# Kernel tuning notes

Measured on AMD Instinct MI355X. Metric: run time of the kernel, lower is better.

The kernel has to match this reference:

```python
import jax, jax.numpy as jnp
import numpy as np

D = 256; NH = 8; NL = 4; NP = 4; DFF = 2048; HD = D // NH
SHAPES = [(64, 64), (32, 32), (16, 16), (8, 8)]
B = 2; LEN = sum(h * w for h, w in SHAPES)


def setup_inputs() -> dict:
    key = jax.random.key(0)
    ks = jax.random.split(key, 12)
    def w(k, shape, s=0.02):
        return jax.random.normal(k, shape, jnp.float32) * s
    starts = np.cumsum([0] + [h * w for h, w in SHAPES[:-1]])
    return {
        "src": jax.random.normal(ks[0], (B, LEN, D), jnp.float32),
        "pos": jax.random.normal(ks[1], (B, LEN, D), jnp.float32) * 0.1,
        "spatial_shapes": jnp.array(SHAPES, dtype=jnp.int32),
        "level_start_index": jnp.array(starts, dtype=jnp.int32),
        "w_value": w(ks[2], (D, D)), "b_value": jnp.zeros((D,), jnp.float32),
        "w_off": w(ks[3], (D, NH * NL * NP * 2)), "b_off": w(ks[4], (NH * NL * NP * 2,), 0.1),
        "w_attn": w(ks[5], (D, NH * NL * NP)), "b_attn": jnp.zeros((NH * NL * NP,), jnp.float32),
        "w_out": w(ks[6], (D, D)), "b_out": jnp.zeros((D,), jnp.float32),
        "w1": w(ks[7], (D, DFF)), "b1": jnp.zeros((DFF,), jnp.float32),
        "w2": w(ks[8], (DFF, D)), "b2": jnp.zeros((D,), jnp.float32),
        "g1": jnp.ones((D,), jnp.float32), "be1": jnp.zeros((D,), jnp.float32),
        "g2": jnp.ones((D,), jnp.float32), "be2": jnp.zeros((D,), jnp.float32),
    }


def _layer_norm(x, g, b):
    mu = jnp.mean(x, -1, keepdims=True)
    v = jnp.var(x, -1, keepdims=True)
    return (x - mu) * jax.lax.rsqrt(v + 1e-5) * g + b


def _reference_points(shapes):
    # torch.linspace(0.5, H-0.5, H)/H == (arange(H)+0.5)/H
    refs = []
    for H, W in shapes:
        ry = (jnp.arange(H, dtype=jnp.float32) + 0.5) / H
        rx = (jnp.arange(W, dtype=jnp.float32) + 0.5) / W
        yy, xx = jnp.meshgrid(ry, rx, indexing='ij')
        refs.append(jnp.stack([xx.ravel(), yy.ravel()], -1))
    return jnp.concatenate(refs, 0)  # (Len, 2) as (x, y)


def _ms_deform_sample(value, loc, shapes):
    # value: (B, Len, NH, HD); loc: (B, Lq, NH, NL, NP, 2) normalized [0,1]
    # Replicates torch grid_sample(bilinear, padding='zeros', align_corners=False).
    Bn, Lq = loc.shape[0], loc.shape[1]
    P = loc.shape[4]
    start = 0
    outs = []
    for lvl, (H, W) in enumerate(shapes):
        v = value[:, start:start + H * W].transpose(0, 2, 1, 3)  # (B, NH, HW, HD)
        start += H * W
        l = loc[:, :, :, lvl]                      # (B, Lq, NH, P, 2)
        x = l[..., 0] * W - 0.5
        y = l[..., 1] * H - 0.5
        x0 = jnp.floor(x); y0 = jnp.floor(y)
        dx = x - x0; dy = y - y0
        x0i = x0.astype(jnp.int32); y0i = y0.astype(jnp.int32)
        acc = None
        for xi, yi, wgt in ((x0i, y0i, (1 - dx) * (1 - dy)),
                            (x0i + 1, y0i, dx * (1 - dy)),
                            (x0i, y0i + 1, (1 - dx) * dy),
                            (x0i + 1, y0i + 1, dx * dy)):
            valid = ((xi >= 0) & (xi < W) & (yi >= 0) & (yi < H)).astype(value.dtype)
            idx = jnp.clip(yi, 0, H - 1) * W + jnp.clip(xi, 0, W - 1)  # (B, Lq, NH, P)
            idx = idx.transpose(0, 2, 1, 3).reshape(Bn, NH, Lq * P)
            g = jnp.take_along_axis(v, idx[..., None], axis=2).reshape(Bn, NH, Lq, P, HD)
            w = (wgt * valid).transpose(0, 2, 1, 3)[..., None]  # (B, NH, Lq, P, 1)
            acc = g * w if acc is None else acc + g * w
        outs.append(acc)  # (B, NH, Lq, P, HD)
    return jnp.stack(outs, 3)  # (B, NH, Lq, NL, NP, HD)


def _forward(src, pos, w_value, b_value, w_off, b_off, w_attn, b_attn,
             w_out, b_out, w1, b1, w2, b2, g1, be1, g2, be2, shapes):
    Bn, Lq, _ = src.shape
    q = src + pos  # with_pos_embed
    value = (src @ w_value + b_value).reshape(Bn, Lq, NH, HD)
    off = (q @ w_off + b_off).reshape(Bn, Lq, NH, NL, NP, 2)
    attn = jax.nn.softmax((q @ w_attn + b_attn).reshape(Bn, Lq, NH, NL * NP), -1)
    attn = attn.reshape(Bn, Lq, NH, NL, NP)
    ref = _reference_points(shapes)  # (Len, 2)
    normalizer = jnp.array([[w_, h_] for h_, w_ in shapes], jnp.float32)  # (NL, 2) = (W, H)
    loc = ref[None, :, None, None, None, :] + off / normalizer[None, None, None, :, None, :]
    sampled = _ms_deform_sample(value, loc, shapes)  # (B, NH, Lq, NL, NP, HD)
    out = jnp.einsum('bqhlp,bhqlpd->bqhd', attn, sampled).reshape(Bn, Lq, D)
    out = out @ w_out + b_out
    x = _layer_norm(src + out, g1, be1)           # residual + norm1
    ff = jax.nn.relu(x @ w1 + b1) @ w2 + b2       # FFN (dropout=0)
    return _layer_norm(x + ff, g2, be2)           # residual + norm2


def reference(src, pos, spatial_shapes, level_start_index, w_value, b_value,
              w_off, b_off, w_attn, b_attn, w_out, b_out, w1, b1, w2, b2,
              g1, be1, g2, be2):
    shapes = [tuple(int(v) for v in s) for s in np.asarray(spatial_shapes)]
    return _forward(src, pos, w_value, b_value, w_off, b_off, w_attn, b_attn,
                    w_out, b_out, w1, b1, w2, b2, g1, be1, g2, be2, shapes)
```

## Files before the change

kernel.cpp:

```cpp
#include <hip/hip_runtime.h>
#include <math.h>

#define D 256
#define NH 8
#define NL 4
#define NP 4
#define DFF 2048
#define HD 32
#define BB 2
#define LEN 5440
#define MROWS (BB * LEN)

typedef __attribute__((ext_vector_type(8))) short short8;
typedef __attribute__((ext_vector_type(4))) float f32x4;
typedef unsigned int uint32;

__device__ __forceinline__ unsigned short f2bf(float f) {
    uint32 u = __float_as_uint(f);
    u += 0x7FFF + ((u >> 16) & 1);
    return (unsigned short)(u >> 16);
}
__device__ __forceinline__ float bf2f(unsigned short h) {
    return __uint_as_float(((uint32)h) << 16);
}
__device__ __forceinline__ uint32 pack2(float a, float b) {
    return (uint32)f2bf(a) | ((uint32)f2bf(b) << 16);
}

__device__ __forceinline__ void swz85(int b, int ncols, int& row, int& col) {
    const int gsz = ncols << 3;
    const int full = 10 * gsz;
    if (b < full) {
        const int g = b / gsz, idx = b - g * gsz;
        row = (g << 3) + (idx & 7);
        col = idx >> 3;
    } else {
        const int idx = b - full;
        row = 80 + idx % 5;
        col = idx / 5;
    }
}

__global__ void prep(const float* __restrict__ w_value, const float* __restrict__ w_off,
                     const float* __restrict__ w_attn, const float* __restrict__ w_out,
                     const float* __restrict__ w1, const float* __restrict__ w2,
                     const float* __restrict__ b_value, const float* __restrict__ b_off,
                     const float* __restrict__ b_attn,
                     unsigned short* __restrict__ wqvT, unsigned short* __restrict__ woT,
                     unsigned short* __restrict__ w1T, unsigned short* __restrict__ w2T,
                     float* __restrict__ bqv) {
    const int blk = blockIdx.x;
    if (blk >= 1248) {
        for (int i = threadIdx.x; i < 640; i += 256)
            bqv[i] = (i < 256) ? b_value[i] : (i < 512 ? b_off[i - 256] : b_attn[i - 512]);
        return;
    }
    const float* W; unsigned short* WT; int K, N, tid;
    if (blk < 64)       { W = w_value; WT = wqvT;             K = 256;  N = 256;  tid = blk; }
    else if (blk < 128) { W = w_off;   WT = wqvT + 256 * 256; K = 256;  N = 256;  tid = blk - 64; }
    else if (blk < 160) { W = w_attn;  WT = wqvT + 512 * 256; K = 256;  N = 128;  tid = blk - 128; }
    else if (blk < 224) { W = w_out;   WT = woT;              K = 256;  N = 256;  tid = blk - 160; }
    else if (blk < 736) { W = w1;      WT = w1T;              K = 256;  N = 2048; tid = blk - 224; }
    else                { W = w2;      WT = w2T;              K = 2048; N = 256;  tid = blk - 736; }
    const int ntx = N >> 5;
    const int nb = (tid % ntx) * 32, kb = (tid / ntx) * 32;

    __shared__ float tile[32][33];
    const int tx = threadIdx.x & 31, ty = threadIdx.x >> 5;
#pragma unroll
    for (int i = 0; i < 32; i += 8)
        tile[ty + i][tx] = W[(size_t)(kb + ty + i) * N + nb + tx];
    __syncthreads();
#pragma unroll
    for (int i = 0; i < 32; i += 8)
        WT[(size_t)(nb + ty + i) * K + kb + tx] = f2bf(tile[tx][ty + i]);
}

__global__ __launch_bounds__(256) void ffn1_gemm(
        const unsigned short* __restrict__ A,
        const unsigned short* __restrict__ BT, const float* __restrict__ bias,
        unsigned short* __restrict__ Cv, int N, int K, int lda, int ldb) {
    __shared__ unsigned short Ash[128][40];
    __shared__ unsigned short Bsh[128][40];

    int rowt, colt;
    swz85(blockIdx.x, N >> 7, rowt, colt);
    const int row0 = rowt * 128, col0 = colt * 128;

    const int t = threadIdx.x;
    const int wave = t >> 6, lane = t & 63;
    const int wr = wave >> 1, wc = wave & 1;
    const int lrow = lane & 15, quad = lane >> 4;
    const int srow = t >> 1;
    const int cb = (t & 1) * 16;

    f32x4 acc[4][4];
#pragma unroll
    for (int i = 0; i < 4; i++)
#pragma unroll
        for (int j = 0; j < 4; j++) acc[i][j] = (f32x4){0.f, 0.f, 0.f, 0.f};

    for (int kb = 0; kb < K; kb += 32) {
        __syncthreads();
        {
            const unsigned short* ap = A + (size_t)(row0 + srow) * lda + kb + cb;
            *(uint4*)&Ash[srow][cb + 0] = *(const uint4*)(ap + 0);
            *(uint4*)&Ash[srow][cb + 8] = *(const uint4*)(ap + 8);
        }
        {
            const unsigned short* bp = BT + (size_t)(col0 + srow) * ldb + kb + cb;
            *(uint4*)&Bsh[srow][cb + 0] = *(const uint4*)(bp + 0);
            *(uint4*)&Bsh[srow][cb + 8] = *(const uint4*)(bp + 8);
        }
        __syncthreads();

        short8 af[4], bfr[4];
#pragma unroll
        for (int mt = 0; mt < 4; mt++)
            af[mt] = *(const short8*)&Ash[wr * 64 + mt * 16 + lrow][quad * 8];
#pragma unroll
        for (int nt = 0; nt < 4; nt++)
            bfr[nt] = *(const short8*)&Bsh[wc * 64 + nt * 16 + lrow][quad * 8];
#pragma unroll
        for (int mt = 0; mt < 4; mt++)
#pragma unroll
            for (int nt = 0; nt < 4; nt++)
                acc[mt][nt] = __builtin_amdgcn_mfma_f32_16x16x32_bf16(
                    af[mt], bfr[nt], acc[mt][nt], 0, 0, 0);
    }

#pragma unroll
    for (int nt = 0; nt < 4; nt++) {
        const int col = col0 + wc * 64 + nt * 16 + lrow;
        const float bv = bias[col];
#pragma unroll
        for (int mt = 0; mt < 4; mt++) {
            f32x4 a = acc[mt][nt];
#pragma unroll
            for (int r = 0; r < 4; r++) {
                const int row = row0 + wr * 64 + mt * 16 + quad * 4 + r;
                Cv[(size_t)row * N + col] = f2bf(fmaxf(a[r] + bv, 0.f));
            }
        }
    }
}

__global__ __launch_bounds__(256) void splitk_gemm(
        const unsigned short* __restrict__ A, const unsigned short* __restrict__ BT,
        float* __restrict__ part, int KC, int lda, int ldb) {
    __shared__ unsigned short Ash[128][40];
    __shared__ unsigned short Bsh[128][40];

    int rowt, cc;
    swz85(blockIdx.x, 4, rowt, cc);
    const int row0 = rowt * 128;
    const int col0 = (cc & 1) * 128;
    const int z = cc >> 1;
    const int koff = z * KC;
    float* __restrict__ C = part + (size_t)z * MROWS * 256;

    const int t = threadIdx.x;
    const int wave = t >> 6, lane = t & 63;
    const int wr = wave >> 1, wc = wave & 1;
    const int lrow = lane & 15, quad = lane >> 4;
    const int srow = t >> 1;
    const int cb = (t & 1) * 16;

    f32x4 acc[4][4];
#pragma unroll
    for (int i = 0; i < 4; i++)
#pragma unroll
        for (int j = 0; j < 4; j++) acc[i][j] = (f32x4){0.f, 0.f, 0.f, 0.f};

    for (int kb = 0; kb < KC; kb += 32) {
        __syncthreads();
        {
            const unsigned short* ap = A + (size_t)(row0 + srow) * lda + koff + kb + cb;
            *(uint4*)&Ash[srow][cb + 0] = *(const uint4*)(ap + 0);
            *(uint4*)&Ash[srow][cb + 8] = *(const uint4*)(ap + 8);
        }
        {
            const unsigned short* bp = BT + (size_t)(col0 + srow) * ldb + koff + kb + cb;
            *(uint4*)&Bsh[srow][cb + 0] = *(const uint4*)(bp + 0);
            *(uint4*)&Bsh[srow][cb + 8] = *(const uint4*)(bp + 8);
        }
        __syncthreads();

        short8 af[4], bfr[4];
#pragma unroll
        for (int mt = 0; mt < 4; mt++)
            af[mt] = *(const short8*)&Ash[wr * 64 + mt * 16 + lrow][quad * 8];
#pragma unroll
        for (int nt = 0; nt < 4; nt++)
            bfr[nt] = *(const short8*)&Bsh[wc * 64 + nt * 16 + lrow][quad * 8];
#pragma unroll
        for (int mt = 0; mt < 4; mt++)
#pragma unroll
            for (int nt = 0; nt < 4; nt++)
                acc[mt][nt] = __builtin_amdgcn_mfma_f32_16x16x32_bf16(
                    af[mt], bfr[nt], acc[mt][nt], 0, 0, 0);
    }

#pragma unroll
    for (int nt = 0; nt < 4; nt++) {
        const int col = col0 + wc * 64 + nt * 16 + lrow;
#pragma unroll
        for (int mt = 0; mt < 4; mt++) {
            f32x4 a = acc[mt][nt];
#pragma unroll
            for (int r = 0; r < 4; r++) {
                const int row = row0 + wr * 64 + mt * 16 + quad * 4 + r;
                C[(size_t)row * 256 + col] = a[r];
            }
        }
    }
}

__global__ __launch_bounds__(256) void qv_gemm(
        const float* __restrict__ src, const float* __restrict__ pos,
        const unsigned short* __restrict__ BT, const float* __restrict__ bias,
        unsigned short* __restrict__ val, float* __restrict__ qout) {
    __shared__ unsigned short Ash[128][40];
    __shared__ unsigned short Bsh[128][40];

    int rowt, colt;
    swz85(blockIdx.x, 5, rowt, colt);
    const int row0 = rowt * 128, col0 = colt * 128;
    const bool addp = (col0 >= 256);

    const int t = threadIdx.x;
    const int wave = t >> 6, lane = t & 63;
    const int wr = wave >> 1, wc = wave & 1;
    const int lrow = lane & 15, quad = lane >> 4;
    const int srow = t >> 1;
    const int cb = (t & 1) * 16;

    f32x4 acc[4][4];
#pragma unroll
    for (int i = 0; i < 4; i++)
#pragma unroll
        for (int j = 0; j < 4; j++) acc[i][j] = (f32x4){0.f, 0.f, 0.f, 0.f};

    for (int kb = 0; kb < 256; kb += 32) {
        __syncthreads();
        {
            const float* ap = src + (size_t)(row0 + srow) * 256 + kb + cb;
            float4 f0 = *(const float4*)(ap + 0);
            float4 f1 = *(const float4*)(ap + 4);
            float4 f2 = *(const float4*)(ap + 8);
            float4 f3 = *(const float4*)(ap + 12);
            if (addp) {
                const float* pp = pos + (size_t)(row0 + srow) * 256 + kb + cb;
                float4 p0 = *(const float4*)(pp + 0);
                float4 p1 = *(const float4*)(pp + 4);
                float4 p2 = *(const float4*)(pp + 8);
                float4 p3 = *(const float4*)(pp + 12);
                f0.x += p0.x; f0.y += p0.y; f0.z += p0.z; f0.w += p0.w;
                f1.x += p1.x; f1.y += p1.y; f1.z += p1.z; f1.w += p1.w;
                f2.x += p2.x; f2.y += p2.y; f2.z += p2.z; f2.w += p2.w;
                f3.x += p3.x; f3.y += p3.y; f3.z += p3.z; f3.w += p3.w;
            }
            uint4 u0 = make_uint4(pack2(f0.x, f0.y), pack2(f0.z, f0.w),
                                  pack2(f1.x, f1.y), pack2(f1.z, f1.w));
            uint4 u1 = make_uint4(pack2(f2.x, f2.y), pack2(f2.z, f2.w),
                                  pack2(f3.x, f3.y), pack2(f3.z, f3.w));
            *(uint4*)&Ash[srow][cb + 0] = u0;
            *(uint4*)&Ash[srow][cb + 8] = u1;
        }
        {
            const unsigned short* bp = BT + (size_t)(col0 + srow) * 256 + kb + cb;
            *(uint4*)&Bsh[srow][cb + 0] = *(const uint4*)(bp + 0);
            *(uint4*)&Bsh[srow][cb + 8] = *(const uint4*)(bp + 8);
        }
        __syncthreads();

        short8 af[4], bfr[4];
#pragma unroll
        for (int mt = 0; mt < 4; mt++)
            af[mt] = *(const short8*)&Ash[wr * 64 + mt * 16 + lrow][quad * 8];
#pragma unroll
        for (int nt = 0; nt < 4; nt++)
            bfr[nt] = *(const short8*)&Bsh[wc * 64 + nt * 16 + lrow][quad * 8];
#pragma unroll
        for (int mt = 0; mt < 4; mt++)
#pragma unroll
            for (int nt = 0; nt < 4; nt++)
                acc[mt][nt] = __builtin_amdgcn_mfma_f32_16x16x32_bf16(
                    af[mt], bfr[nt], acc[mt][nt], 0, 0, 0);
    }

#pragma unroll
    for (int nt = 0; nt < 4; nt++) {
        const int col = col0 + wc * 64 + nt * 16 + lrow;
        const float bv = bias[col];
#pragma unroll
        for (int mt = 0; mt < 4; mt++) {
            f32x4 a = acc[mt][nt];
#pragma unroll
            for (int r = 0; r < 4; r++) {
                const int row = row0 + wr * 64 + mt * 16 + quad * 4 + r;
                float v = a[r] + bv;
                if (col < 256)
                    val[(size_t)row * 256 + col] = f2bf(v);
                else
                    qout[(size_t)row * 384 + (col - 256)] = v;
            }
        }
    }
}

__global__ void sampler(const unsigned short* __restrict__ val, const float* __restrict__ qout,
                        unsigned short* __restrict__ out) {
    __shared__ __align__(16) int   sIdx[128][4];
    __shared__ __align__(16) float sW[128][4];
    const int bq = blockIdx.x;
    const int b = bq / LEN, q = bq % LEN;
    const int t = threadIdx.x;

    if (t < 128) {
        const int h = t >> 4, p = t & 15;
        const int l = p >> 2;

        float refx, refy;
        if (q < 4096) {
            int rq = q >> 6, cq = q & 63;
            refx = (cq + 0.5f) * (1.0f / 64.0f);
            refy = (rq + 0.5f) * (1.0f / 64.0f);
        } else if (q < 5120) {
            int qq = q - 4096;
            int rq = qq >> 5, cq = qq & 31;
            refx = (cq + 0.5f) * (1.0f / 32.0f);
            refy = (rq + 0.5f) * (1.0f / 32.0f);
        } else if (q < 5376) {
            int qq = q - 5120;
            int rq = qq >> 4, cq = qq & 15;
            refx = (cq + 0.5f) * (1.0f / 16.0f);
            refy = (rq + 0.5f) * (1.0f / 16.0f);
        } else {
            int qq = q - 5376;
            int rq = qq >> 3, cq = qq & 7;
            refx = (cq + 0.5f) * (1.0f / 8.0f);
            refy = (rq + 0.5f) * (1.0f / 8.0f);
        }

        float lv = qout[(size_t)bq * 384 + 256 + t];
        float mx = lv;
#pragma unroll
        for (int o = 1; o < 16; o <<= 1) mx = fmaxf(mx, __shfl_xor(mx, o, 16));
        float e = expf(lv - mx);
        float s = e;
#pragma unroll
        for (int o = 1; o < 16; o <<= 1) s += __shfl_xor(s, o, 16);
        const float aw = e / s;

        const float ox = qout[(size_t)bq * 384 + h * 32 + p * 2 + 0];
        const float oy = qout[(size_t)bq * 384 + h * 32 + p * 2 + 1];

        const int LST[4] = {0, 4096, 5120, 5376};
        const int WW = 64 >> l;
        const float rw = 1.0f / (float)WW;

        float x = (refx + ox * rw) * (float)WW - 0.5f;
        float y = (refy + oy * rw) * (float)WW - 0.5f;
        float x0f = floorf(x), y0f = floorf(y);
        float dx = x - x0f, dy = y - y0f;
        int x0 = (int)x0f, y0 = (int)y0f;

        const int base = (b * LEN + LST[l]) * 256 + h * 32;
        int4 iv; float4 wv;
        {
            int xs[2] = {x0, x0 + 1}, ys[2] = {y0, y0 + 1};
            float wx[2] = {1.f - dx, dx}, wy[2] = {1.f - dy, dy};
            int ic[4]; float wc4[4];
#pragma unroll
            for (int cy = 0; cy < 2; cy++)
#pragma unroll
                for (int cx = 0; cx < 2; cx++) {
                    int xi = xs[cx], yi = ys[cy];
                    bool vld = (xi >= 0) && (xi < WW) && (yi >= 0) && (yi < WW);
                    int xc = min(max(xi, 0), WW - 1);
                    int yc = min(max(yi, 0), WW - 1);
                    ic[cy * 2 + cx] = base + (yc * WW + xc) * 256;
                    wc4[cy * 2 + cx] = vld ? wx[cx] * wy[cy] * aw : 0.f;
                }
            iv = make_int4(ic[0], ic[1], ic[2], ic[3]);
            wv = make_float4(wc4[0], wc4[1], wc4[2], wc4[3]);
        }
        *(int4*)&sIdx[t][0] = iv;
        *(float4*)&sW[t][0] = wv;
    }
    __syncthreads();

    const int h = t >> 5, d = t & 31;
    const unsigned short* vald = val + d;
    float acc = 0.f;
#pragma unroll 4
    for (int p = 0; p < 16; p++) {
        const int r = h * 16 + p;
        int4 iv = *(const int4*)&sIdx[r][0];
        float4 wv = *(const float4*)&sW[r][0];
        acc += bf2f(vald[iv.x]) * wv.x;
        acc += bf2f(vald[iv.y]) * wv.y;
        acc += bf2f(vald[iv.z]) * wv.z;
        acc += bf2f(vald[iv.w]) * wv.w;
    }
    out[(size_t)bq * D + h * HD + d] = f2bf(acc);
}

__global__ void add_ln2(const float* __restrict__ p0, const float* __restrict__ p1,
                        const float* __restrict__ bias, const float* __restrict__ rsd,
                        const float* __restrict__ g, const float* __restrict__ be,
                        float* __restrict__ out, unsigned short* __restrict__ out16) {
    __shared__ float r1[4], r2[4];
    const int row = blockIdx.x, t = threadIdx.x;
    const size_t i = (size_t)row * D + t;
    const float v = p0[i] + p1[i] + bias[t] + rsd[i];
    float s1 = v, s2 = v * v;
#pragma unroll
    for (int o = 32; o > 0; o >>= 1) {
        s1 += __shfl_down(s1, o, 64);
        s2 += __shfl_down(s2, o, 64);
    }
    if ((t & 63) == 0) { r1[t >> 6] = s1; r2[t >> 6] = s2; }
    __syncthreads();
    float su = r1[0] + r1[1] + r1[2] + r1[3];
    float sq = r2[0] + r2[1] + r2[2] + r2[3];
    float mean = su * (1.0f / D);
    float var = fmaxf(sq * (1.0f / D) - mean * mean, 0.f);
    const float o = (v - mean) * rsqrtf(var + 1e-5f) * g[t] + be[t];
    out[i] = o;
    if (out16) out16[i] = f2bf(o);
}

extern "C" void kernel_launch(void* const* d_in, const int* in_sizes, int n_in,
                              void* d_out, int out_size, void* d_ws, size_t ws_size,
                              hipStream_t stream) {
    const float* src     = (const float*)d_in[0];
    const float* pos     = (const float*)d_in[1];
    const float* w_value = (const float*)d_in[4];
    const float* b_value = (const float*)d_in[5];
    const float* w_off   = (const float*)d_in[6];
    const float* b_off   = (const float*)d_in[7];
    const float* w_attn  = (const float*)d_in[8];
    const float* b_attn  = (const float*)d_in[9];
    const float* w_out   = (const float*)d_in[10];
    const float* b_out   = (const float*)d_in[11];
    const float* w1      = (const float*)d_in[12];
    const float* b1      = (const float*)d_in[13];
    const float* w2      = (const float*)d_in[14];
    const float* b2      = (const float*)d_in[15];
    const float* g1      = (const float*)d_in[16];
    const float* be1     = (const float*)d_in[17];
    const float* g2      = (const float*)d_in[18];
    const float* be2     = (const float*)d_in[19];
    float* out = (float*)d_out;

    size_t off = 0;
    auto alloc = [&](size_t bytes) -> char* {
        char* p = (char*)d_ws + off;
        off += (bytes + 255) & ~(size_t)255;
        return p;
    };
    unsigned short* wqvT = (unsigned short*)alloc((size_t)640 * 256 * 2);
    unsigned short* woT  = (unsigned short*)alloc(256 * 256 * 2);
    unsigned short* w1T  = (unsigned short*)alloc((size_t)2048 * 256 * 2);
    unsigned short* w2T  = (unsigned short*)alloc((size_t)256 * 2048 * 2);
    float* bqv           = (float*)alloc(640 * 4);

    float* qout          = (float*)alloc((size_t)MROWS * 384 * 4);
    unsigned short* val  = (unsigned short*)alloc((size_t)MROWS * 256 * 2);
    unsigned short* attn = (unsigned short*)alloc((size_t)MROWS * 256 * 2);
    unsigned short* hb   = (unsigned short*)alloc((size_t)MROWS * 2048 * 2);
    float* xbuf          = (float*)alloc((size_t)MROWS * 256 * 4);
    unsigned short* xb16 = (unsigned short*)alloc((size_t)MROWS * 256 * 2);
    float* part          = (float*)alloc((size_t)2 * MROWS * 256 * 4);

    prep<<<1249, 256, 0, stream>>>(w_value, w_off, w_attn, w_out, w1, w2,
                                   b_value, b_off, b_attn, wqvT, woT, w1T, w2T, bqv);

    qv_gemm<<<425, 256, 0, stream>>>(src, pos, wqvT, bqv, val, qout);
    sampler<<<MROWS, 256, 0, stream>>>(val, qout, attn);
    splitk_gemm<<<340, 256, 0, stream>>>(attn, woT, part, 128, 256, 256);
    add_ln2<<<MROWS, 256, 0, stream>>>(part, part + (size_t)MROWS * 256, b_out, src,
                                       g1, be1, xbuf, xb16);

    ffn1_gemm<<<1360, 256, 0, stream>>>(xb16, w1T, b1, hb, 2048, 256, 256, 256);
    splitk_gemm<<<340, 256, 0, stream>>>(hb, w2T, part, 1024, 2048, 2048);
    add_ln2<<<MROWS, 256, 0, stream>>>(part, part + (size_t)MROWS * 256, b2, xbuf,
                                       g2, be2, out, nullptr);
}
```

Baseline: 242.5 us.

## Register-prefetch next K tile in GEMMs and raise FFN2 split-K to four

Result: faster. 225.9 us (-6.8%).

```diff
diff --git a/kernel.cpp b/kernel.cpp
--- a/kernel.cpp
+++ b/kernel.cpp
@@ -94,25 +94,31 @@
     const int srow = t >> 1;
     const int cb = (t & 1) * 16;
 
+    const unsigned short* ap = A + (size_t)(row0 + srow) * lda + cb;
+    const unsigned short* bp = BT + (size_t)(col0 + srow) * ldb + cb;
+
     f32x4 acc[4][4];
 #pragma unroll
     for (int i = 0; i < 4; i++)
 #pragma unroll
         for (int j = 0; j < 4; j++) acc[i][j] = (f32x4){0.f, 0.f, 0.f, 0.f};
+
+    uint4 ra0 = *(const uint4*)(ap + 0), ra1 = *(const uint4*)(ap + 8);
+    uint4 rb0 = *(const uint4*)(bp + 0), rb1 = *(const uint4*)(bp + 8);
 
     for (int kb = 0; kb < K; kb += 32) {
         __syncthreads();
-        {
-            const unsigned short* ap = A + (size_t)(row0 + srow) * lda + kb + cb;
-            *(uint4*)&Ash[srow][cb + 0] = *(const uint4*)(ap + 0);
-            *(uint4*)&Ash[srow][cb + 8] = *(const uint4*)(ap + 8);
-        }
-        {
-            const unsigned short* bp = BT + (size_t)(col0 + srow) * ldb + kb + cb;
-            *(uint4*)&Bsh[srow][cb + 0] = *(const uint4*)(bp + 0);
-            *(uint4*)&Bsh[srow][cb + 8] = *(const uint4*)(bp + 8);
-        }
+        *(uint4*)&Ash[srow][cb + 0] = ra0;
+        *(uint4*)&Ash[srow][cb + 8] = ra1;
+        *(uint4*)&Bsh[srow][cb + 0] = rb0;
+        *(uint4*)&Bsh[srow][cb + 8] = rb1;
         __syncthreads();
+        if (kb + 32 < K) {
+            ra0 = *(const uint4*)(ap + kb + 32 + 0);
+            ra1 = *(const uint4*)(ap + kb + 32 + 8);
+            rb0 = *(const uint4*)(bp + kb + 32 + 0);
+            rb1 = *(const uint4*)(bp + kb + 32 + 8);
+        }
 
         short8 af[4], bfr[4];
 #pragma unroll
@@ -145,6 +151,7 @@
     }
 }
 
+template <int NZ>
 __global__ __launch_bounds__(256) void splitk_gemm(
         const unsigned short* __restrict__ A, const unsigned short* __restrict__ BT,
         float* __restrict__ part, int KC, int lda, int ldb) {
@@ -152,7 +159,7 @@
     __shared__ unsigned short Bsh[128][40];
 
     int rowt, cc;
-    swz85(blockIdx.x, 4, rowt, cc);
+    swz85(blockIdx.x, 2 * NZ, rowt, cc);
     const int row0 = rowt * 128;
     const int col0 = (cc & 1) * 128;
     const int z = cc >> 1;
@@ -166,25 +173,31 @@
     const int srow = t >> 1;
     const int cb = (t & 1) * 16;
 
+    const unsigned short* ap = A + (size_t)(row0 + srow) * lda + koff + cb;
+    const unsigned short* bp = BT + (size_t)(col0 + srow) * ldb + koff + cb;
+
     f32x4 acc[4][4];
 #pragma unroll
     for (int i = 0; i < 4; i++)
 #pragma unroll
         for (int j = 0; j < 4; j++) acc[i][j] = (f32x4){0.f, 0.f, 0.f, 0.f};
+
+    uint4 ra0 = *(const uint4*)(ap + 0), ra1 = *(const uint4*)(ap + 8);
+    uint4 rb0 = *(const uint4*)(bp + 0), rb1 = *(const uint4*)(bp + 8);
 
     for (int kb = 0; kb < KC; kb += 32) {
         __syncthreads();
-        {
-            const unsigned short* ap = A + (size_t)(row0 + srow) * lda + koff + kb + cb;
-            *(uint4*)&Ash[srow][cb + 0] = *(const uint4*)(ap + 0);
-            *(uint4*)&Ash[srow][cb + 8] = *(const uint4*)(ap + 8);
-        }
-        {
-            const unsigned short* bp = BT + (size_t)(col0 + srow) * ldb + koff + kb + cb;
-            *(uint4*)&Bsh[srow][cb + 0] = *(const uint4*)(bp + 0);
-            *(uint4*)&Bsh[srow][cb + 8] = *(const uint4*)(bp + 8);
-        }
+        *(uint4*)&Ash[srow][cb + 0] = ra0;
+        *(uint4*)&Ash[srow][cb + 8] = ra1;
+        *(uint4*)&Bsh[srow][cb + 0] = rb0;
+        *(uint4*)&Bsh[srow][cb + 8] = rb1;
         __syncthreads();
+        if (kb + 32 < KC) {
+            ra0 = *(const uint4*)(ap + kb + 32 + 0);
+            ra1 = *(const uint4*)(ap + kb + 32 + 8);
+            rb0 = *(const uint4*)(bp + kb + 32 + 0);
+            rb1 = *(const uint4*)(bp + kb + 32 + 8);
+        }
 
         short8 af[4], bfr[4];
 #pragma unroll
@@ -235,30 +248,35 @@
     const int srow = t >> 1;
     const int cb = (t & 1) * 16;
 
+    const float* ap = src + (size_t)(row0 + srow) * 256 + cb;
+    const float* pp = pos + (size_t)(row0 + srow) * 256 + cb;
+    const unsigned short* bp = BT + (size_t)(col0 + srow) * 256 + cb;
+
     f32x4 acc[4][4];
 #pragma unroll
     for (int i = 0; i < 4; i++)
 #pragma unroll
         for (int j = 0; j < 4; j++) acc[i][j] = (f32x4){0.f, 0.f, 0.f, 0.f};
+
+    float4 fa[4]; float4 fp[4]; uint4 rb0, rb1;
+#pragma unroll
+    for (int j = 0; j < 4; j++) fa[j] = *(const float4*)(ap + 4 * j);
+    if (addp) {
+#pragma unroll
+        for (int j = 0; j < 4; j++) fp[j] = *(const float4*)(pp + 4 * j);
+    }
+    rb0 = *(const uint4*)(bp + 0);
+    rb1 = *(const uint4*)(bp + 8);
 
     for (int kb = 0; kb < 256; kb += 32) {
         __syncthreads();
         {
-            const float* ap = src + (size_t)(row0 + srow) * 256 + kb + cb;
-            float4 f0 = *(const float4*)(ap + 0);
-            float4 f1 = *(const float4*)(ap + 4);
-            float4 f2 = *(const float4*)(ap + 8);
-            float4 f3 = *(const float4*)(ap + 12);
+            float4 f0 = fa[0], f1 = fa[1], f2 = fa[2], f3 = fa[3];
             if (addp) {
-                const float* pp = pos + (size_t)(row0 + srow) * 256 + kb + cb;
-                float4 p0 = *(const float4*)(pp + 0);
-                float4 p1 = *(const float4*)(pp + 4);
-                float4 p2 = *(const float4*)(pp + 8);
-                float4 p3 = *(const float4*)(pp + 12);
-                f0.x += p0.x; f0.y += p0.y; f0.z += p0.z; f0.w += p0.w;
-                f1.x += p1.x; f1.y += p1.y; f1.z += p1.z; f1.w += p1.w;
-                f2.x += p2.x; f2.y += p2.y; f2.z += p2.z; f2.w += p2.w;
-                f3.x += p3.x; f3.y += p3.y; f3.z += p3.z; f3.w += p3.w;
+                f0.x += fp[0].x; f0.y += fp[0].y; f0.z += fp[0].z; f0.w += fp[0].w;
+                f1.x += fp[1].x; f1.y += fp[1].y; f1.z += fp[1].z; f1.w += fp[1].w;
+                f2.x += fp[2].x; f2.y += fp[2].y; f2.z += fp[2].z; f2.w += fp[2].w;
+                f3.x += fp[3].x; f3.y += fp[3].y; f3.z += fp[3].z; f3.w += fp[3].w;
             }
             uint4 u0 = make_uint4(pack2(f0.x, f0.y), pack2(f0.z, f0.w),
                                   pack2(f1.x, f1.y), pack2(f1.z, f1.w));
@@ -266,13 +284,20 @@
                                   pack2(f3.x, f3.y), pack2(f3.z, f3.w));
             *(uint4*)&Ash[srow][cb + 0] = u0;
             *(uint4*)&Ash[srow][cb + 8] = u1;
-        }
-        {
-            const unsigned short* bp = BT + (size_t)(col0 + srow) * 256 + kb + cb;
-            *(uint4*)&Bsh[srow][cb + 0] = *(const uint4*)(bp + 0);
-            *(uint4*)&Bsh[srow][cb + 8] = *(const uint4*)(bp + 8);
+            *(uint4*)&Bsh[srow][cb + 0] = rb0;
+            *(uint4*)&Bsh[srow][cb + 8] = rb1;
         }
         __syncthreads();
+        if (kb + 32 < 256) {
+#pragma unroll
+            for (int j = 0; j < 4; j++) fa[j] = *(const float4*)(ap + kb + 32 + 4 * j);
+            if (addp) {
+#pragma unroll
+                for (int j = 0; j < 4; j++) fp[j] = *(const float4*)(pp + kb + 32 + 4 * j);
+            }
+            rb0 = *(const uint4*)(bp + kb + 32 + 0);
+            rb1 = *(const uint4*)(bp + kb + 32 + 8);
+        }
 
         short8 af[4], bfr[4];
 #pragma unroll
@@ -407,14 +432,17 @@
     out[(size_t)bq * D + h * HD + d] = f2bf(acc);
 }
 
-__global__ void add_ln2(const float* __restrict__ p0, const float* __restrict__ p1,
-                        const float* __restrict__ bias, const float* __restrict__ rsd,
+template <int NPART>
+__global__ void add_lnN(const float* __restrict__ part, const float* __restrict__ bias,
+                        const float* __restrict__ rsd,
                         const float* __restrict__ g, const float* __restrict__ be,
                         float* __restrict__ out, unsigned short* __restrict__ out16) {
     __shared__ float r1[4], r2[4];
     const int row = blockIdx.x, t = threadIdx.x;
     const size_t i = (size_t)row * D + t;
-    const float v = p0[i] + p1[i] + bias[t] + rsd[i];
+    float v = bias[t] + rsd[i];
+#pragma unroll
+    for (int z = 0; z < NPART; z++) v += part[(size_t)z * MROWS * 256 + i];
     float s1 = v, s2 = v * v;
 #pragma unroll
     for (int o = 32; o > 0; o >>= 1) {
@@ -473,19 +501,17 @@
     unsigned short* hb   = (unsigned short*)alloc((size_t)MROWS * 2048 * 2);
     float* xbuf          = (float*)alloc((size_t)MROWS * 256 * 4);
     unsigned short* xb16 = (unsigned short*)alloc((size_t)MROWS * 256 * 2);
-    float* part          = (float*)alloc((size_t)2 * MROWS * 256 * 4);
+    float* part          = (float*)alloc((size_t)4 * MROWS * 256 * 4);
 
     prep<<<1249, 256, 0, stream>>>(w_value, w_off, w_attn, w_out, w1, w2,
                                    b_value, b_off, b_attn, wqvT, woT, w1T, w2T, bqv);
 
     qv_gemm<<<425, 256, 0, stream>>>(src, pos, wqvT, bqv, val, qout);
     sampler<<<MROWS, 256, 0, stream>>>(val, qout, attn);
-    splitk_gemm<<<340, 256, 0, stream>>>(attn, woT, part, 128, 256, 256);
-    add_ln2<<<MROWS, 256, 0, stream>>>(part, part + (size_t)MROWS * 256, b_out, src,
-                                       g1, be1, xbuf, xb16);
+    splitk_gemm<2><<<340, 256, 0, stream>>>(attn, woT, part, 128, 256, 256);
+    add_lnN<2><<<MROWS, 256, 0, stream>>>(part, b_out, src, g1, be1, xbuf, xb16);
 
     ffn1_gemm<<<1360, 256, 0, stream>>>(xb16, w1T, b1, hb, 2048, 256, 256, 256);
-    splitk_gemm<<<340, 256, 0, stream>>>(hb, w2T, part, 1024, 2048, 2048);
-    add_ln2<<<MROWS, 256, 0, stream>>>(part, part + (size_t)MROWS * 256, b2, xbuf,
-                                       g2, be2, out, nullptr);
-}
+    splitk_gemm<4><<<680, 256, 0, stream>>>(hb, w2T, part, 512, 2048, 2048);
+    add_lnN<4><<<MROWS, 256, 0, stream>>>(part, b2, xbuf, g2, be2, out, nullptr);
+}
```
